# Optimization experiments

Measured on AMD Instinct MI355X. Metric: run time of the kernel, lower is better.

## Reference

```python
import jax, jax.numpy as jnp
import numpy as np

B, A, H, L = 4096, 4096, 768, 4  # batch, num_atoms, hidden_dim, antecedent_len


def setup_inputs() -> dict:
    key = jax.random.key(0)
    ks = jax.random.split(key, 10)
    s = 0.02
    cls = jax.random.normal(ks[0], (B, H), jnp.float32)
    x_ = jax.random.bernoulli(ks[1], 0.5, (B, A)).astype(jnp.float32)
    gru_w_ih = jax.random.normal(ks[2], (3 * H, H), jnp.float32) * s
    gru_w_hh = jax.random.normal(ks[3], (3 * H, H), jnp.float32) * s
    gru_b_ih = jax.random.normal(ks[4], (3 * H,), jnp.float32) * s
    gru_b_hh = jax.random.normal(ks[5], (3 * H,), jnp.float32) * s
    head_w = jax.random.normal(ks[6], (A, H), jnp.float32) * s
    head_b = jax.random.normal(ks[7], (A,), jnp.float32) * s
    ae_weight = jax.random.normal(ks[8], (A, H), jnp.float32) * s
    return {"cls": cls, "x_": x_, "gru_w_ih": gru_w_ih, "gru_w_hh": gru_w_hh,
            "gru_b_ih": gru_b_ih, "gru_b_hh": gru_b_hh, "head_w": head_w,
            "head_b": head_b, "ae_weight": ae_weight}


def _gru_step(x, h, w_ih, w_hh, b_ih, b_hh):
    # torch GRU gate order: r, z, n
    gi = x @ w_ih.T + b_ih          # [B, 3H]
    gh = h @ w_hh.T + b_hh
    i_r, i_z, i_n = jnp.split(gi, 3, axis=-1)
    h_r, h_z, h_n = jnp.split(gh, 3, axis=-1)
    r = jax.nn.sigmoid(i_r + h_r)
    z = jax.nn.sigmoid(i_z + h_z)
    n = jnp.tanh(i_n + r * h_n)
    return (1.0 - z) * n + z * h


def reference(cls, x_, gru_w_ih, gru_w_hh, gru_b_ih, gru_b_hh, head_w, head_b, ae_weight):
    key = jax.random.key(42)
    mask = x_
    h = jnp.zeros_like(cls)
    cur_input = cls
    max_index = None
    rows = jnp.arange(B)
    probs = []
    for j in range(L):
        h = _gru_step(cur_input, h, gru_w_ih, gru_w_hh, gru_b_ih, gru_b_hh)
        out = h @ head_w.T + head_b  # [B, A]  (dropout = identity in eval)
        # filtered_softmax mask update (mutations persist across steps)
        if j == 0:
            empty = jnp.sum(mask, axis=-1) == 0.0
            mask = mask.at[:, 0].set(jnp.where(empty, 1.0, mask[:, 0]))
        else:
            mask = jnp.where((max_index == 0)[:, None], 0.0, mask)
            mask = mask.at[:, 0].set(1.0)
        logits = jnp.where(mask > 0, out, -jnp.inf)
        # hard gumbel-softmax, tau=1 (straight-through)
        key, sub = jax.random.split(key)
        g = jax.random.gumbel(sub, logits.shape, logits.dtype)
        y_soft = jax.nn.softmax(logits + g, axis=1)
        idx = jnp.argmax(y_soft, axis=1)
        y_hard = jax.nn.one_hot(idx, A, dtype=y_soft.dtype)
        prob = y_hard + y_soft - jax.lax.stop_gradient(y_soft)
        max_index = idx
        # scatter zeros at the selected atom (remove from candidate set)
        mask = mask.at[rows, idx].set(0.0)
        probs.append(prob)
        atom_wsum = prob @ jax.lax.stop_gradient(ae_weight)  # [B, H]
        cur_input = cls + atom_wsum
    return jnp.stack(probs, axis=1)  # [B, L, A]
```

## Files before the change

kernel.cpp:

```cpp
#include <hip/hip_runtime.h>
#include <cstdint>
#include <cstddef>
#include <math.h>


#define KB 4096
#define KA 4096
#define KH 768
#define KL 4

typedef __attribute__((ext_vector_type(8))) short bf16x8;
typedef __attribute__((ext_vector_type(4))) float f32x4;

__host__ __device__ inline unsigned rotl32(unsigned x, int d) {
  return (x << d) | (x >> (32 - d));
}

__host__ __device__ inline void tf2x32(unsigned k0, unsigned k1,
                                       unsigned x0, unsigned x1,
                                       unsigned& o0, unsigned& o1) {
  unsigned ks2 = k0 ^ k1 ^ 0x1BD11BDAu;
  x0 += k0; x1 += k1;
#define TF_R(r) { x0 += x1; x1 = rotl32(x1, (r)); x1 ^= x0; }
  TF_R(13) TF_R(15) TF_R(26) TF_R(6)
  x0 += k1;  x1 += ks2 + 1u;
  TF_R(17) TF_R(29) TF_R(16) TF_R(24)
  x0 += ks2; x1 += k0 + 2u;
  TF_R(13) TF_R(15) TF_R(26) TF_R(6)
  x0 += k0;  x1 += k1 + 3u;
  TF_R(17) TF_R(29) TF_R(16) TF_R(24)
  x0 += k1;  x1 += ks2 + 4u;
  TF_R(13) TF_R(15) TF_R(26) TF_R(6)
  x0 += ks2; x1 += k0 + 5u;
#undef TF_R
  o0 = x0; o1 = x1;
}

__device__ inline ushort f2bf(float f) {
  unsigned u = __float_as_uint(f);
  unsigned r = (u + 0x7fffu + ((u >> 16) & 1u)) >> 16;
  return (ushort)r;
}
__device__ inline float bf2f(ushort h) {
  return __uint_as_float(((unsigned)h) << 16);
}

__device__ inline float gumbel_at(unsigned s0, unsigned s1, unsigned ctr) {
  unsigned o0, o1;
  tf2x32(s0, s1, 0u, ctr, o0, o1);
  unsigned bits = o0 ^ o1;
  float f = __uint_as_float((bits >> 9) | 0x3f800000u) - 1.0f;
  const float TINY = 1.17549435e-38f;
  float u = fmaxf(TINY, f + TINY);
  return -logf(-logf(u));
}

__global__ __launch_bounds__(256) void gemm3_nt(
    const ushort* __restrict__ Ahi, const ushort* __restrict__ Alo,
    const ushort* __restrict__ Bhi, const ushort* __restrict__ Blo,
    float* __restrict__ C, long long ldc) {
  __shared__ ushort smem[4 * 128 * 64];
  const int tid = threadIdx.x;
  const int wave = tid >> 6;
  const int lane = tid & 63;
  const long long bm = (long long)blockIdx.y * 128;
  const long long bn = (long long)blockIdx.x * 128;
  const int wm = (wave & 1) * 64;
  const int wn = (wave >> 1) * 64;

  f32x4 acc[4][4];
#pragma unroll
  for (int i = 0; i < 4; ++i)
#pragma unroll
    for (int j = 0; j < 4; ++j) acc[i][j] = (f32x4){0.f, 0.f, 0.f, 0.f};

  const int r = lane >> 3;
  const int csrc = (lane & 7) ^ r;
  const int m15 = lane & 15;
  const int kg = (lane >> 4) & 3;

  for (int kt = 0; kt < 12; ++kt) {
    const int k0 = kt * 64;
#pragma unroll
    for (int s = 0; s < 4; ++s) {
      const int m0 = wave * 32 + s * 8;
      const long long arow = (bm + m0 + r) * KH + k0 + csrc * 8;
      const long long brow = (bn + m0 + r) * KH + k0 + csrc * 8;
      __builtin_amdgcn_global_load_lds(
          (const __attribute__((address_space(1))) void*)(Ahi + arow),
          (__attribute__((address_space(3))) void*)&smem[0 * 8192 + m0 * 64], 16, 0, 0);
      __builtin_amdgcn_global_load_lds(
          (const __attribute__((address_space(1))) void*)(Alo + arow),
          (__attribute__((address_space(3))) void*)&smem[1 * 8192 + m0 * 64], 16, 0, 0);
      __builtin_amdgcn_global_load_lds(
          (const __attribute__((address_space(1))) void*)(Bhi + brow),
          (__attribute__((address_space(3))) void*)&smem[2 * 8192 + m0 * 64], 16, 0, 0);
      __builtin_amdgcn_global_load_lds(
          (const __attribute__((address_space(1))) void*)(Blo + brow),
          (__attribute__((address_space(3))) void*)&smem[3 * 8192 + m0 * 64], 16, 0, 0);
    }
    __syncthreads();
#pragma unroll
    for (int ks = 0; ks < 2; ++ks) {
      bf16x8 ah[4], al[4], bh[4], bl[4];
#pragma unroll
      for (int i = 0; i < 4; ++i) {
        const int m = wm + i * 16 + m15;
        const int slot = (ks * 4 + kg) ^ (lane & 7);
        ah[i] = *(const bf16x8*)&smem[0 * 8192 + m * 64 + slot * 8];
        al[i] = *(const bf16x8*)&smem[1 * 8192 + m * 64 + slot * 8];
        const int n = wn + i * 16 + m15;
        bh[i] = *(const bf16x8*)&smem[2 * 8192 + n * 64 + slot * 8];
        bl[i] = *(const bf16x8*)&smem[3 * 8192 + n * 64 + slot * 8];
      }
#pragma unroll
      for (int i = 0; i < 4; ++i)
#pragma unroll
        for (int j = 0; j < 4; ++j) {
          acc[i][j] = __builtin_amdgcn_mfma_f32_16x16x32_bf16(ah[i], bh[j], acc[i][j], 0, 0, 0);
          acc[i][j] = __builtin_amdgcn_mfma_f32_16x16x32_bf16(ah[i], bl[j], acc[i][j], 0, 0, 0);
          acc[i][j] = __builtin_amdgcn_mfma_f32_16x16x32_bf16(al[i], bh[j], acc[i][j], 0, 0, 0);
        }
    }
    __syncthreads();
  }
  const int rq = (lane >> 4) * 4;
#pragma unroll
  for (int i = 0; i < 4; ++i)
#pragma unroll
    for (int j = 0; j < 4; ++j) {
      const long long n = bn + wn + j * 16 + m15;
#pragma unroll
      for (int rg = 0; rg < 4; ++rg) {
        const long long m = bm + wm + i * 16 + rq + rg;
        C[m * ldc + n] = acc[i][j][rg];
      }
    }
}

__global__ __launch_bounds__(256) void gemm1_nt(
    const ushort* __restrict__ Ahi, const ushort* __restrict__ Bhi,
    float* __restrict__ C, long long ldc) {
  __shared__ ushort smem[2 * 128 * 64];
  const int tid = threadIdx.x;
  const int wave = tid >> 6;
  const int lane = tid & 63;
  const long long bm = (long long)blockIdx.y * 128;
  const long long bn = (long long)blockIdx.x * 128;
  const int wm = (wave & 1) * 64;
  const int wn = (wave >> 1) * 64;

  f32x4 acc[4][4];
#pragma unroll
  for (int i = 0; i < 4; ++i)
#pragma unroll
    for (int j = 0; j < 4; ++j) acc[i][j] = (f32x4){0.f, 0.f, 0.f, 0.f};

  const int r = lane >> 3;
  const int csrc = (lane & 7) ^ r;
  const int m15 = lane & 15;
  const int kg = (lane >> 4) & 3;

  for (int kt = 0; kt < 12; ++kt) {
    const int k0 = kt * 64;
#pragma unroll
    for (int s = 0; s < 4; ++s) {
      const int m0 = wave * 32 + s * 8;
      const long long arow = (bm + m0 + r) * KH + k0 + csrc * 8;
      const long long brow = (bn + m0 + r) * KH + k0 + csrc * 8;
      __builtin_amdgcn_global_load_lds(
          (const __attribute__((address_space(1))) void*)(Ahi + arow),
          (__attribute__((address_space(3))) void*)&smem[0 * 8192 + m0 * 64], 16, 0, 0);
      __builtin_amdgcn_global_load_lds(
          (const __attribute__((address_space(1))) void*)(Bhi + brow),
          (__attribute__((address_space(3))) void*)&smem[1 * 8192 + m0 * 64], 16, 0, 0);
    }
    __syncthreads();
#pragma unroll
    for (int ks = 0; ks < 2; ++ks) {
      bf16x8 ah[4], bh[4];
#pragma unroll
      for (int i = 0; i < 4; ++i) {
        const int m = wm + i * 16 + m15;
        const int slot = (ks * 4 + kg) ^ (lane & 7);
        ah[i] = *(const bf16x8*)&smem[0 * 8192 + m * 64 + slot * 8];
        const int n = wn + i * 16 + m15;
        bh[i] = *(const bf16x8*)&smem[1 * 8192 + n * 64 + slot * 8];
      }
#pragma unroll
      for (int i = 0; i < 4; ++i)
#pragma unroll
        for (int j = 0; j < 4; ++j)
          acc[i][j] = __builtin_amdgcn_mfma_f32_16x16x32_bf16(ah[i], bh[j], acc[i][j], 0, 0, 0);
    }
    __syncthreads();
  }
  const int rq = (lane >> 4) * 4;
#pragma unroll
  for (int i = 0; i < 4; ++i)
#pragma unroll
    for (int j = 0; j < 4; ++j) {
      const long long n = bn + wn + j * 16 + m15;
#pragma unroll
      for (int rg = 0; rg < 4; ++rg) {
        const long long m = bm + wm + i * 16 + rq + rg;
        C[m * ldc + n] = acc[i][j][rg];
      }
    }
}

#define CUM1 442368
#define CUM2 884736
#define CUM3 1671168
#define CUM4 2457600
#define CUM5 3244032
#define PREP_CONV_BLOCKS 12672

__global__ void prep(const float* __restrict__ w_ih, const float* __restrict__ w_hh,
                     const float* __restrict__ head_w, const float* __restrict__ cls,
                     const float* __restrict__ ae_w,
                     ushort* __restrict__ WihHi, ushort* __restrict__ WihLo,
                     ushort* __restrict__ WhhHi, ushort* __restrict__ WhhLo,
                     ushort* __restrict__ HwHi, ushort* __restrict__ CAhi,
                     ushort* __restrict__ CAlo) {
  const int i = blockIdx.x * 256 + threadIdx.x;
  const float* src; ushort* dhi; ushort* dlo; int base; int split; int ofs = 0;
  if (i < CUM1)      { src = w_ih;   dhi = WihHi; dlo = WihLo; base = 0;    split = 1; }
  else if (i < CUM2) { src = w_hh;   dhi = WhhHi; dlo = WhhLo; base = CUM1; split = 1; }
  else if (i < CUM3) { src = head_w; dhi = HwHi;  dlo = 0;     base = CUM2; split = 0; }
  else if (i < CUM4) { src = cls;    dhi = CAhi;  dlo = CAlo;  base = CUM3; split = 1; }
  else               { src = ae_w;   dhi = CAhi;  dlo = CAlo;  base = CUM4; split = 1; ofs = 786432; }
  const int k = i - base;
  float4 v = ((const float4*)src)[k];
  ushort4 h;
  h.x = f2bf(v.x); h.y = f2bf(v.y); h.z = f2bf(v.z); h.w = f2bf(v.w);
  ((ushort4*)dhi)[ofs + k] = h;
  if (split) {
    ushort4 l;
    l.x = f2bf(v.x - bf2f(h.x)); l.y = f2bf(v.y - bf2f(h.y));
    l.z = f2bf(v.z - bf2f(h.z)); l.w = f2bf(v.w - bf2f(h.w));
    ((ushort4*)dlo)[ofs + k] = l;
  }
}

__global__ void gru_gate2(const float* __restrict__ PAE, const float* __restrict__ Gh,
                          const int* __restrict__ idxbuf,
                          const float* __restrict__ b_ih, const float* __restrict__ b_hh,
                          float* __restrict__ h, ushort* __restrict__ hHi,
                          ushort* __restrict__ hLo, int first) {
  int i = blockIdx.x * 256 + threadIdx.x;
  int b = i / KH, c = i - b * KH;
  const float* gp = PAE + (size_t)b * (3 * KH);
  float ir = gp[c], iz = gp[c + KH], in_ = gp[c + 2 * KH];
  float hr = b_hh[c], hz = b_hh[c + KH], hn = b_hh[c + 2 * KH];
  float hp = 0.f;
  if (!first) {
    const float* ga = PAE + ((size_t)KB + idxbuf[b]) * (3 * KH);
    ir += ga[c]; iz += ga[c + KH]; in_ += ga[c + 2 * KH];
    const float* gh = Gh + (size_t)b * (3 * KH);
    hr += gh[c]; hz += gh[c + KH]; hn += gh[c + 2 * KH];
    hp = h[i];
  }
  ir += b_ih[c]; iz += b_ih[c + KH]; in_ += b_ih[c + 2 * KH];
  float rr = 1.f / (1.f + expf(-(ir + hr)));
  float z = 1.f / (1.f + expf(-(iz + hz)));
  float n = tanhf(in_ + rr * hn);
  float hv = (1.f - z) * n + z * hp;
  h[i] = hv;
  ushort hh = f2bf(hv);
  hHi[i] = hh;
  hLo[i] = f2bf(hv - bf2f(hh));
}

__global__ __launch_bounds__(256) void sample_step(
    float* __restrict__ out, const float* __restrict__ head_b,
    const float* __restrict__ x_, unsigned char* __restrict__ mask,
    int* __restrict__ idxbuf, const float* __restrict__ hbuf,
    const float* __restrict__ head_w, int j, unsigned s0, unsigned s1) {
  const int b = blockIdx.x;
  const int tid = threadIdx.x;
  float* orow = out + ((size_t)b * KL + j) * KA;
  unsigned char* mrow = mask + (size_t)b * KA;
  const float* xrow = x_ + (size_t)b * KA;
  __shared__ float sv[256];
  __shared__ int si[256];
  __shared__ int scand[16];
  __shared__ float srefined[16];
  __shared__ int scnt;
  __shared__ int ssel;
  const float EPS = 0.01f;

  if (tid == 0) scnt = 0;

  int idx_prev = 0;
  if (j > 0) idx_prev = idxbuf[b];

  int empty = 0;
  if (j == 0) {
    int cnt = 0;
#pragma unroll
    for (int t = 0; t < 16; ++t) cnt += (xrow[tid + (t << 8)] != 0.f) ? 1 : 0;
    si[tid] = cnt;
    __syncthreads();
    for (int s = 128; s > 0; s >>= 1) {
      if (tid < s) si[tid] += si[tid + s];
      __syncthreads();
    }
    empty = (si[0] == 0);
    __syncthreads();
  }

  float vreg[16];
  unsigned mbits = 0;
  float lmax = -INFINITY;
#pragma unroll
  for (int t = 0; t < 16; ++t) {
    int a = tid + (t << 8);
    int m;
    if (j == 0) {
      m = (xrow[a] != 0.f) ? 1 : 0;
      if (empty && a == 0) m = 1;
    } else {
      m = mrow[a];
      if (idx_prev == 0) m = 0;
      if (a == 0) m = 1;
    }
    float v = -INFINITY;
    if (m) {
      float g = gumbel_at(s0, s1, (unsigned)(b * KA + a));
      v = orow[a] + head_b[a] + g;
      mbits |= (1u << t);
    }
    vreg[t] = v;
    lmax = fmaxf(lmax, v);
  }
  sv[tid] = lmax;
  __syncthreads();
  for (int s = 128; s > 0; s >>= 1) {
    if (tid < s) sv[tid] = fmaxf(sv[tid], sv[tid + s]);
    __syncthreads();
  }
  const float vmax = sv[0];

  const float thresh = vmax - EPS;
#pragma unroll
  for (int t = 0; t < 16; ++t) {
    if (vreg[t] >= thresh) {
      int slot = atomicAdd(&scnt, 1);
      if (slot < 16) scand[slot] = tid + (t << 8);
    }
  }
  __syncthreads();
  const int ncand = min(scnt, 16);

  {
    const int wv = tid >> 6;
    const int lane = tid & 63;
    const float4* h4 = (const float4*)(hbuf + (size_t)b * KH);
    for (int t = wv; t < ncand; t += 4) {
      const int a = scand[t];
      const float4* w4 = (const float4*)(head_w + (size_t)a * KH);
      float sum = 0.f;
#pragma unroll
      for (int u = 0; u < 3; ++u) {
        float4 hv = h4[lane + u * 64];
        float4 wv4 = w4[lane + u * 64];
        sum = fmaf(hv.x, wv4.x, sum);
        sum = fmaf(hv.y, wv4.y, sum);
        sum = fmaf(hv.z, wv4.z, sum);
        sum = fmaf(hv.w, wv4.w, sum);
      }
#pragma unroll
      for (int off = 32; off > 0; off >>= 1) sum += __shfl_down(sum, off);
      if (lane == 0) {
        float g = gumbel_at(s0, s1, (unsigned)(b * KA + a));
        srefined[t] = sum + head_b[a] + g;
      }
    }
  }
  __syncthreads();

  if (tid == 0) {
    float best = -INFINITY;
    int bsel = KA;
    for (int t = 0; t < ncand; ++t) {
      float v = srefined[t];
      int a = scand[t];
      if (v > best || (v == best && a < bsel)) { best = v; bsel = a; }
    }
    ssel = bsel;
  }
  __syncthreads();
  const int sel = ssel;

#pragma unroll
  for (int t = 0; t < 16; ++t) {
    int a = tid + (t << 8);
    int m = (mbits >> t) & 1;
    if (a == sel) m = 0;
    mrow[a] = (unsigned char)m;
    orow[a] = (a == sel) ? 1.f : 0.f;
  }
  if (tid == 0) idxbuf[b] = sel;
}

extern "C" void kernel_launch(void* const* d_in, const int* in_sizes, int n_in,
                              void* d_out, int out_size, void* d_ws, size_t ws_size,
                              hipStream_t stream) {
  const float* cls    = (const float*)d_in[0];
  const float* x_     = (const float*)d_in[1];
  const float* w_ih   = (const float*)d_in[2];
  const float* w_hh   = (const float*)d_in[3];
  const float* b_ih   = (const float*)d_in[4];
  const float* b_hh   = (const float*)d_in[5];
  const float* head_w = (const float*)d_in[6];
  const float* head_b = (const float*)d_in[7];
  const float* ae_w   = (const float*)d_in[8];
  float* out = (float*)d_out;

  char* p = (char*)d_ws;
  ushort* CAhi  = (ushort*)p; p += (size_t)2 * KB * KH * 2;
  ushort* CAlo  = (ushort*)p; p += (size_t)2 * KB * KH * 2;
  ushort* WihHi = (ushort*)p; p += (size_t)3 * KH * KH * 2;
  ushort* WihLo = (ushort*)p; p += (size_t)3 * KH * KH * 2;
  ushort* WhhHi = (ushort*)p; p += (size_t)3 * KH * KH * 2;
  ushort* WhhLo = (ushort*)p; p += (size_t)3 * KH * KH * 2;
  ushort* HwHi  = (ushort*)p; p += (size_t)KA * KH * 2;
  ushort* hHi   = (ushort*)p; p += (size_t)KB * KH * 2;
  ushort* hLo   = (ushort*)p; p += (size_t)KB * KH * 2;
  float*  hbuf  = (float*)p;  p += (size_t)KB * KH * 4;
  float*  PAE   = (float*)p;  p += (size_t)2 * KB * 3 * KH * 4;
  float*  Gh    = (float*)p;  p += (size_t)KB * 3 * KH * 4;
  unsigned char* mask = (unsigned char*)p; p += (size_t)KB * KA;
  int* idxbuf = (int*)p; p += (size_t)KB * 4;

  unsigned key0 = 0u, key1 = 42u;
  unsigned sub0[KL], sub1[KL];
  for (int j = 0; j < KL; ++j) {
    unsigned n0, n1, t0, t1;
    tf2x32(key0, key1, 0u, 0u, n0, n1);
    tf2x32(key0, key1, 0u, 1u, t0, t1);
    sub0[j] = t0; sub1[j] = t1;
    key0 = n0; key1 = n1;
  }

  prep<<<PREP_CONV_BLOCKS, 256, 0, stream>>>(
      w_ih, w_hh, head_w, cls, ae_w,
      WihHi, WihLo, WhhHi, WhhLo, HwHi, CAhi, CAlo);
  gemm3_nt<<<dim3(3 * KH / 128, 2 * KB / 128), 256, 0, stream>>>(
      CAhi, CAlo, WihHi, WihLo, PAE, 3 * KH);

  for (int j = 0; j < KL; ++j) {
    if (j > 0)
      gemm3_nt<<<dim3(3 * KH / 128, KB / 128), 256, 0, stream>>>(
          hHi, hLo, WhhHi, WhhLo, Gh, 3 * KH);
    gru_gate2<<<KB * KH / 256, 256, 0, stream>>>(PAE, Gh, idxbuf, b_ih, b_hh,
                                                 hbuf, hHi, hLo, j == 0);
    gemm1_nt<<<dim3(KA / 128, KB / 128), 256, 0, stream>>>(
        hHi, HwHi, out + (size_t)j * KA, (long long)KL * KA);
    sample_step<<<KB, 256, 0, stream>>>(out, head_b, x_, mask, idxbuf, hbuf,
                                        head_w, j, sub0[j], sub1[j]);
  }
}
```

Baseline: 1.154 ms.

## Halve GEMM K-tile, vectorize GRU gate and sampler, move empty-row check to prep

The GEMM kernels now use a K tile of 32 instead of 64, with a new XOR swizzle. This halves LDS use, which may allow more blocks per CU, but doubles the number of barrier iterations. Register pressure drops because only B fragments are held while A is loaded per row. The GRU gate kernel and the sampling kernel now use float4 and packed-byte vectorized accesses. The per-row empty-mask reduction moves out of the step-0 sampler into extra blocks of the prep kernel.

After: 1.055 ms. -8.6%, faster.

```diff
diff --git a/kernel.cpp b/kernel.cpp
--- a/kernel.cpp
+++ b/kernel.cpp
@@ -55,11 +55,16 @@
   return -logf(-logf(u));
 }
 
+#define GLDS(gp, lp) \
+  __builtin_amdgcn_global_load_lds( \
+      (const __attribute__((address_space(1))) void*)(gp), \
+      (__attribute__((address_space(3))) void*)(lp), 16, 0, 0)
+
 __global__ __launch_bounds__(256) void gemm3_nt(
     const ushort* __restrict__ Ahi, const ushort* __restrict__ Alo,
     const ushort* __restrict__ Bhi, const ushort* __restrict__ Blo,
     float* __restrict__ C, long long ldc) {
-  __shared__ ushort smem[4 * 128 * 64];
+  __shared__ ushort smem[4 * 128 * 32];
   const int tid = threadIdx.x;
   const int wave = tid >> 6;
   const int lane = tid & 63;
@@ -74,53 +79,44 @@
 #pragma unroll
     for (int j = 0; j < 4; ++j) acc[i][j] = (f32x4){0.f, 0.f, 0.f, 0.f};
 
-  const int r = lane >> 3;
-  const int csrc = (lane & 7) ^ r;
+  const int r = lane >> 2;
+  const int cs = lane & 3;
+  const int csrc = cs ^ ((r & 3) ^ ((r >> 2) & 3));
   const int m15 = lane & 15;
   const int kg = (lane >> 4) & 3;
-
-  for (int kt = 0; kt < 12; ++kt) {
-    const int k0 = kt * 64;
-#pragma unroll
-    for (int s = 0; s < 4; ++s) {
-      const int m0 = wave * 32 + s * 8;
+  const int slot = kg ^ ((m15 & 3) ^ ((m15 >> 2) & 3));
+
+  for (int kt = 0; kt < 24; ++kt) {
+    const int k0 = kt * 32;
+#pragma unroll
+    for (int s = 0; s < 2; ++s) {
+      const int m0 = wave * 32 + s * 16;
       const long long arow = (bm + m0 + r) * KH + k0 + csrc * 8;
       const long long brow = (bn + m0 + r) * KH + k0 + csrc * 8;
-      __builtin_amdgcn_global_load_lds(
-          (const __attribute__((address_space(1))) void*)(Ahi + arow),
-          (__attribute__((address_space(3))) void*)&smem[0 * 8192 + m0 * 64], 16, 0, 0);
-      __builtin_amdgcn_global_load_lds(
-          (const __attribute__((address_space(1))) void*)(Alo + arow),
-          (__attribute__((address_space(3))) void*)&smem[1 * 8192 + m0 * 64], 16, 0, 0);
-      __builtin_amdgcn_global_load_lds(
-          (const __attribute__((address_space(1))) void*)(Bhi + brow),
-          (__attribute__((address_space(3))) void*)&smem[2 * 8192 + m0 * 64], 16, 0, 0);
-      __builtin_amdgcn_global_load_lds(
-          (const __attribute__((address_space(1))) void*)(Blo + brow),
-          (__attribute__((address_space(3))) void*)&smem[3 * 8192 + m0 * 64], 16, 0, 0);
+      GLDS(Ahi + arow, &smem[0 * 4096 + m0 * 32]);
+      GLDS(Alo + arow, &smem[1 * 4096 + m0 * 32]);
+      GLDS(Bhi + brow, &smem[2 * 4096 + m0 * 32]);
+      GLDS(Blo + brow, &smem[3 * 4096 + m0 * 32]);
     }
     __syncthreads();
-#pragma unroll
-    for (int ks = 0; ks < 2; ++ks) {
-      bf16x8 ah[4], al[4], bh[4], bl[4];
-#pragma unroll
-      for (int i = 0; i < 4; ++i) {
-        const int m = wm + i * 16 + m15;
-        const int slot = (ks * 4 + kg) ^ (lane & 7);
-        ah[i] = *(const bf16x8*)&smem[0 * 8192 + m * 64 + slot * 8];
-        al[i] = *(const bf16x8*)&smem[1 * 8192 + m * 64 + slot * 8];
-        const int n = wn + i * 16 + m15;
-        bh[i] = *(const bf16x8*)&smem[2 * 8192 + n * 64 + slot * 8];
-        bl[i] = *(const bf16x8*)&smem[3 * 8192 + n * 64 + slot * 8];
-      }
-#pragma unroll
-      for (int i = 0; i < 4; ++i)
-#pragma unroll
-        for (int j = 0; j < 4; ++j) {
-          acc[i][j] = __builtin_amdgcn_mfma_f32_16x16x32_bf16(ah[i], bh[j], acc[i][j], 0, 0, 0);
-          acc[i][j] = __builtin_amdgcn_mfma_f32_16x16x32_bf16(ah[i], bl[j], acc[i][j], 0, 0, 0);
-          acc[i][j] = __builtin_amdgcn_mfma_f32_16x16x32_bf16(al[i], bh[j], acc[i][j], 0, 0, 0);
-        }
+    bf16x8 bh[4], bl[4];
+#pragma unroll
+    for (int jj = 0; jj < 4; ++jj) {
+      const int n = wn + jj * 16 + m15;
+      bh[jj] = *(const bf16x8*)&smem[2 * 4096 + n * 32 + slot * 8];
+      bl[jj] = *(const bf16x8*)&smem[3 * 4096 + n * 32 + slot * 8];
+    }
+#pragma unroll
+    for (int i = 0; i < 4; ++i) {
+      const int m = wm + i * 16 + m15;
+      bf16x8 ah = *(const bf16x8*)&smem[0 * 4096 + m * 32 + slot * 8];
+      bf16x8 al = *(const bf16x8*)&smem[1 * 4096 + m * 32 + slot * 8];
+#pragma unroll
+      for (int jj = 0; jj < 4; ++jj) {
+        acc[i][jj] = __builtin_amdgcn_mfma_f32_16x16x32_bf16(ah, bh[jj], acc[i][jj], 0, 0, 0);
+        acc[i][jj] = __builtin_amdgcn_mfma_f32_16x16x32_bf16(ah, bl[jj], acc[i][jj], 0, 0, 0);
+        acc[i][jj] = __builtin_amdgcn_mfma_f32_16x16x32_bf16(al, bh[jj], acc[i][jj], 0, 0, 0);
+      }
     }
     __syncthreads();
   }
@@ -141,7 +137,7 @@
 __global__ __launch_bounds__(256) void gemm1_nt(
     const ushort* __restrict__ Ahi, const ushort* __restrict__ Bhi,
     float* __restrict__ C, long long ldc) {
-  __shared__ ushort smem[2 * 128 * 64];
+  __shared__ ushort smem[2 * 128 * 32];
   const int tid = threadIdx.x;
   const int wave = tid >> 6;
   const int lane = tid & 63;
@@ -156,42 +152,37 @@
 #pragma unroll
     for (int j = 0; j < 4; ++j) acc[i][j] = (f32x4){0.f, 0.f, 0.f, 0.f};
 
-  const int r = lane >> 3;
-  const int csrc = (lane & 7) ^ r;
+  const int r = lane >> 2;
+  const int cs = lane & 3;
+  const int csrc = cs ^ ((r & 3) ^ ((r >> 2) & 3));
   const int m15 = lane & 15;
   const int kg = (lane >> 4) & 3;
-
-  for (int kt = 0; kt < 12; ++kt) {
-    const int k0 = kt * 64;
-#pragma unroll
-    for (int s = 0; s < 4; ++s) {
-      const int m0 = wave * 32 + s * 8;
+  const int slot = kg ^ ((m15 & 3) ^ ((m15 >> 2) & 3));
+
+  for (int kt = 0; kt < 24; ++kt) {
+    const int k0 = kt * 32;
+#pragma unroll
+    for (int s = 0; s < 2; ++s) {
+      const int m0 = wave * 32 + s * 16;
       const long long arow = (bm + m0 + r) * KH + k0 + csrc * 8;
       const long long brow = (bn + m0 + r) * KH + k0 + csrc * 8;
-      __builtin_amdgcn_global_load_lds(
-          (const __attribute__((address_space(1))) void*)(Ahi + arow),
-          (__attribute__((address_space(3))) void*)&smem[0 * 8192 + m0 * 64], 16, 0, 0);
-      __builtin_amdgcn_global_load_lds(
-          (const __attribute__((address_space(1))) void*)(Bhi + brow),
-          (__attribute__((address_space(3))) void*)&smem[1 * 8192 + m0 * 64], 16, 0, 0);
+      GLDS(Ahi + arow, &smem[0 * 4096 + m0 * 32]);
+      GLDS(Bhi + brow, &smem[1 * 4096 + m0 * 32]);
     }
     __syncthreads();
-#pragma unroll
-    for (int ks = 0; ks < 2; ++ks) {
-      bf16x8 ah[4], bh[4];
-#pragma unroll
-      for (int i = 0; i < 4; ++i) {
-        const int m = wm + i * 16 + m15;
-        const int slot = (ks * 4 + kg) ^ (lane & 7);
-        ah[i] = *(const bf16x8*)&smem[0 * 8192 + m * 64 + slot * 8];
-        const int n = wn + i * 16 + m15;
-        bh[i] = *(const bf16x8*)&smem[1 * 8192 + n * 64 + slot * 8];
-      }
-#pragma unroll
-      for (int i = 0; i < 4; ++i)
-#pragma unroll
-        for (int j = 0; j < 4; ++j)
-          acc[i][j] = __builtin_amdgcn_mfma_f32_16x16x32_bf16(ah[i], bh[j], acc[i][j], 0, 0, 0);
+    bf16x8 bh[4];
+#pragma unroll
+    for (int jj = 0; jj < 4; ++jj) {
+      const int n = wn + jj * 16 + m15;
+      bh[jj] = *(const bf16x8*)&smem[1 * 4096 + n * 32 + slot * 8];
+    }
+#pragma unroll
+    for (int i = 0; i < 4; ++i) {
+      const int m = wm + i * 16 + m15;
+      bf16x8 ah = *(const bf16x8*)&smem[0 * 4096 + m * 32 + slot * 8];
+#pragma unroll
+      for (int jj = 0; jj < 4; ++jj)
+        acc[i][jj] = __builtin_amdgcn_mfma_f32_16x16x32_bf16(ah, bh[jj], acc[i][jj], 0, 0, 0);
     }
     __syncthreads();
   }
@@ -218,28 +209,49 @@
 
 __global__ void prep(const float* __restrict__ w_ih, const float* __restrict__ w_hh,
                      const float* __restrict__ head_w, const float* __restrict__ cls,
-                     const float* __restrict__ ae_w,
+                     const float* __restrict__ ae_w, const float* __restrict__ x_,
                      ushort* __restrict__ WihHi, ushort* __restrict__ WihLo,
                      ushort* __restrict__ WhhHi, ushort* __restrict__ WhhLo,
                      ushort* __restrict__ HwHi, ushort* __restrict__ CAhi,
-                     ushort* __restrict__ CAlo) {
-  const int i = blockIdx.x * 256 + threadIdx.x;
-  const float* src; ushort* dhi; ushort* dlo; int base; int split; int ofs = 0;
-  if (i < CUM1)      { src = w_ih;   dhi = WihHi; dlo = WihLo; base = 0;    split = 1; }
-  else if (i < CUM2) { src = w_hh;   dhi = WhhHi; dlo = WhhLo; base = CUM1; split = 1; }
-  else if (i < CUM3) { src = head_w; dhi = HwHi;  dlo = 0;     base = CUM2; split = 0; }
-  else if (i < CUM4) { src = cls;    dhi = CAhi;  dlo = CAlo;  base = CUM3; split = 1; }
-  else               { src = ae_w;   dhi = CAhi;  dlo = CAlo;  base = CUM4; split = 1; ofs = 786432; }
-  const int k = i - base;
-  float4 v = ((const float4*)src)[k];
-  ushort4 h;
-  h.x = f2bf(v.x); h.y = f2bf(v.y); h.z = f2bf(v.z); h.w = f2bf(v.w);
-  ((ushort4*)dhi)[ofs + k] = h;
-  if (split) {
-    ushort4 l;
-    l.x = f2bf(v.x - bf2f(h.x)); l.y = f2bf(v.y - bf2f(h.y));
-    l.z = f2bf(v.z - bf2f(h.z)); l.w = f2bf(v.w - bf2f(h.w));
-    ((ushort4*)dlo)[ofs + k] = l;
+                     ushort* __restrict__ CAlo, unsigned char* __restrict__ empty) {
+  const int blk = blockIdx.x;
+  const int tid = threadIdx.x;
+  if (blk < PREP_CONV_BLOCKS) {
+    const int i = blk * 256 + tid;
+    const float* src; ushort* dhi; ushort* dlo; int base; int split; int ofs = 0;
+    if (i < CUM1)      { src = w_ih;   dhi = WihHi; dlo = WihLo; base = 0;    split = 1; }
+    else if (i < CUM2) { src = w_hh;   dhi = WhhHi; dlo = WhhLo; base = CUM1; split = 1; }
+    else if (i < CUM3) { src = head_w; dhi = HwHi;  dlo = 0;     base = CUM2; split = 0; }
+    else if (i < CUM4) { src = cls;    dhi = CAhi;  dlo = CAlo;  base = CUM3; split = 1; }
+    else               { src = ae_w;   dhi = CAhi;  dlo = CAlo;  base = CUM4; split = 1; ofs = 786432; }
+    const int k = i - base;
+    float4 v = ((const float4*)src)[k];
+    ushort4 h;
+    h.x = f2bf(v.x); h.y = f2bf(v.y); h.z = f2bf(v.z); h.w = f2bf(v.w);
+    ((ushort4*)dhi)[ofs + k] = h;
+    if (split) {
+      ushort4 l;
+      l.x = f2bf(v.x - bf2f(h.x)); l.y = f2bf(v.y - bf2f(h.y));
+      l.z = f2bf(v.z - bf2f(h.z)); l.w = f2bf(v.w - bf2f(h.w));
+      ((ushort4*)dlo)[ofs + k] = l;
+    }
+  } else {
+    const int row = blk - PREP_CONV_BLOCKS;
+    __shared__ int scnt[256];
+    const float4* xr = (const float4*)(x_ + (size_t)row * KA);
+    int cnt = 0;
+#pragma unroll
+    for (int k = 0; k < 4; ++k) {
+      float4 v = xr[tid + (k << 8)];
+      cnt += (v.x != 0.f) + (v.y != 0.f) + (v.z != 0.f) + (v.w != 0.f);
+    }
+    scnt[tid] = cnt;
+    __syncthreads();
+    for (int s = 128; s > 0; s >>= 1) {
+      if (tid < s) scnt[tid] += scnt[tid + s];
+      __syncthreads();
+    }
+    if (tid == 0) empty[row] = (scnt[0] == 0) ? 1 : 0;
   }
 }
 
@@ -248,42 +260,55 @@
                           const float* __restrict__ b_ih, const float* __restrict__ b_hh,
                           float* __restrict__ h, ushort* __restrict__ hHi,
                           ushort* __restrict__ hLo, int first) {
-  int i = blockIdx.x * 256 + threadIdx.x;
-  int b = i / KH, c = i - b * KH;
-  const float* gp = PAE + (size_t)b * (3 * KH);
-  float ir = gp[c], iz = gp[c + KH], in_ = gp[c + 2 * KH];
-  float hr = b_hh[c], hz = b_hh[c + KH], hn = b_hh[c + 2 * KH];
-  float hp = 0.f;
+  int i4 = blockIdx.x * 256 + threadIdx.x;
+  int b = i4 / (KH / 4);
+  int c4 = i4 - b * (KH / 4);
+  const f32x4* gp = (const f32x4*)(PAE + (size_t)b * (3 * KH));
+  f32x4 ir = gp[c4], iz = gp[c4 + 192], inn = gp[c4 + 384];
+  const f32x4* bi = (const f32x4*)b_ih;
+  const f32x4* bhh = (const f32x4*)b_hh;
+  f32x4 hr = bhh[c4], hz = bhh[c4 + 192], hn = bhh[c4 + 384];
+  f32x4 hp = (f32x4){0.f, 0.f, 0.f, 0.f};
   if (!first) {
-    const float* ga = PAE + ((size_t)KB + idxbuf[b]) * (3 * KH);
-    ir += ga[c]; iz += ga[c + KH]; in_ += ga[c + 2 * KH];
-    const float* gh = Gh + (size_t)b * (3 * KH);
-    hr += gh[c]; hz += gh[c + KH]; hn += gh[c + 2 * KH];
-    hp = h[i];
-  }
-  ir += b_ih[c]; iz += b_ih[c + KH]; in_ += b_ih[c + 2 * KH];
-  float rr = 1.f / (1.f + expf(-(ir + hr)));
-  float z = 1.f / (1.f + expf(-(iz + hz)));
-  float n = tanhf(in_ + rr * hn);
-  float hv = (1.f - z) * n + z * hp;
-  h[i] = hv;
-  ushort hh = f2bf(hv);
-  hHi[i] = hh;
-  hLo[i] = f2bf(hv - bf2f(hh));
+    const f32x4* ga = (const f32x4*)(PAE + ((size_t)KB + idxbuf[b]) * (3 * KH));
+    ir += ga[c4]; iz += ga[c4 + 192]; inn += ga[c4 + 384];
+    const f32x4* gh = (const f32x4*)(Gh + (size_t)b * (3 * KH));
+    hr += gh[c4]; hz += gh[c4 + 192]; hn += gh[c4 + 384];
+    hp = ((const f32x4*)h)[i4];
+  }
+  ir += bi[c4]; iz += bi[c4 + 192]; inn += bi[c4 + 384];
+  f32x4 hv;
+  ushort4 hh, hl;
+  ushort* hhp = &hh.x;
+  ushort* hlp = &hl.x;
+#pragma unroll
+  for (int e = 0; e < 4; ++e) {
+    float rr = 1.f / (1.f + expf(-(ir[e] + hr[e])));
+    float z = 1.f / (1.f + expf(-(iz[e] + hz[e])));
+    float n = tanhf(inn[e] + rr * hn[e]);
+    float v = (1.f - z) * n + z * hp[e];
+    hv[e] = v;
+    ushort hb = f2bf(v);
+    hhp[e] = hb;
+    hlp[e] = f2bf(v - bf2f(hb));
+  }
+  ((f32x4*)h)[i4] = hv;
+  ((ushort4*)hHi)[i4] = hh;
+  ((ushort4*)hLo)[i4] = hl;
 }
 
 __global__ __launch_bounds__(256) void sample_step(
     float* __restrict__ out, const float* __restrict__ head_b,
     const float* __restrict__ x_, unsigned char* __restrict__ mask,
     int* __restrict__ idxbuf, const float* __restrict__ hbuf,
-    const float* __restrict__ head_w, int j, unsigned s0, unsigned s1) {
+    const float* __restrict__ head_w, const unsigned char* __restrict__ empty,
+    int j, unsigned s0, unsigned s1) {
   const int b = blockIdx.x;
   const int tid = threadIdx.x;
   float* orow = out + ((size_t)b * KL + j) * KA;
   unsigned char* mrow = mask + (size_t)b * KA;
   const float* xrow = x_ + (size_t)b * KA;
   __shared__ float sv[256];
-  __shared__ int si[256];
   __shared__ int scand[16];
   __shared__ float srefined[16];
   __shared__ int scnt;
@@ -292,47 +317,49 @@
 
   if (tid == 0) scnt = 0;
 
-  int idx_prev = 0;
-  if (j > 0) idx_prev = idxbuf[b];
-
-  int empty = 0;
-  if (j == 0) {
-    int cnt = 0;
-#pragma unroll
-    for (int t = 0; t < 16; ++t) cnt += (xrow[tid + (t << 8)] != 0.f) ? 1 : 0;
-    si[tid] = cnt;
-    __syncthreads();
-    for (int s = 128; s > 0; s >>= 1) {
-      if (tid < s) si[tid] += si[tid + s];
-      __syncthreads();
-    }
-    empty = (si[0] == 0);
-    __syncthreads();
-  }
+  const int idx_prev = (j > 0) ? idxbuf[b] : 0;
+  const int emp = (j == 0) ? empty[b] : 0;
 
   float vreg[16];
   unsigned mbits = 0;
   float lmax = -INFINITY;
-#pragma unroll
-  for (int t = 0; t < 16; ++t) {
-    int a = tid + (t << 8);
-    int m;
+  const float4* orow4 = (const float4*)orow;
+  const float4* xrow4 = (const float4*)xrow;
+  const unsigned* mrow4 = (const unsigned*)mrow;
+  const float4* hb4 = (const float4*)head_b;
+#pragma unroll
+  for (int k = 0; k < 4; ++k) {
+    const int ci = tid + (k << 8);
+    const int abase = ci * 4;
+    float4 lv = orow4[ci];
+    float4 hbv = hb4[ci];
+    float lvv[4] = {lv.x + hbv.x, lv.y + hbv.y, lv.z + hbv.z, lv.w + hbv.w};
+    float xvv[4] = {0.f, 0.f, 0.f, 0.f};
+    unsigned mword = 0;
     if (j == 0) {
-      m = (xrow[a] != 0.f) ? 1 : 0;
-      if (empty && a == 0) m = 1;
+      float4 xv = xrow4[ci];
+      xvv[0] = xv.x; xvv[1] = xv.y; xvv[2] = xv.z; xvv[3] = xv.w;
     } else {
-      m = mrow[a];
-      if (idx_prev == 0) m = 0;
-      if (a == 0) m = 1;
-    }
-    float v = -INFINITY;
-    if (m) {
-      float g = gumbel_at(s0, s1, (unsigned)(b * KA + a));
-      v = orow[a] + head_b[a] + g;
-      mbits |= (1u << t);
-    }
-    vreg[t] = v;
-    lmax = fmaxf(lmax, v);
+      mword = mrow4[ci];
+    }
+#pragma unroll
+    for (int e = 0; e < 4; ++e) {
+      const int a = abase + e;
+      int m;
+      if (j == 0) {
+        m = (xvv[e] != 0.f) || (emp && a == 0);
+      } else {
+        m = (a == 0) || (idx_prev != 0 && ((mword >> (8 * e)) & 0xffu));
+      }
+      float v = -INFINITY;
+      if (m) {
+        float g = gumbel_at(s0, s1, (unsigned)(b * KA + a));
+        v = lvv[e] + g;
+        mbits |= (1u << (k * 4 + e));
+      }
+      vreg[k * 4 + e] = v;
+      lmax = fmaxf(lmax, v);
+    }
   }
   sv[tid] = lmax;
   __syncthreads();
@@ -344,12 +371,14 @@
 
   const float thresh = vmax - EPS;
 #pragma unroll
-  for (int t = 0; t < 16; ++t) {
-    if (vreg[t] >= thresh) {
-      int slot = atomicAdd(&scnt, 1);
-      if (slot < 16) scand[slot] = tid + (t << 8);
-    }
-  }
+  for (int k = 0; k < 4; ++k)
+#pragma unroll
+    for (int e = 0; e < 4; ++e) {
+      if (vreg[k * 4 + e] >= thresh) {
+        int slot = atomicAdd(&scnt, 1);
+        if (slot < 16) scand[slot] = (tid + (k << 8)) * 4 + e;
+      }
+    }
   __syncthreads();
   const int ncand = min(scnt, 16);
 
@@ -394,12 +423,22 @@
   const int sel = ssel;
 
 #pragma unroll
-  for (int t = 0; t < 16; ++t) {
-    int a = tid + (t << 8);
-    int m = (mbits >> t) & 1;
-    if (a == sel) m = 0;
-    mrow[a] = (unsigned char)m;
-    orow[a] = (a == sel) ? 1.f : 0.f;
+  for (int k = 0; k < 4; ++k) {
+    const int ci = tid + (k << 8);
+    const int abase = ci * 4;
+    unsigned mw = 0;
+    float4 ov;
+    float* ovp = &ov.x;
+#pragma unroll
+    for (int e = 0; e < 4; ++e) {
+      const int a = abase + e;
+      int m = (mbits >> (k * 4 + e)) & 1;
+      if (a == sel) m = 0;
+      mw |= ((unsigned)m) << (8 * e);
+      ovp[e] = (a == sel) ? 1.f : 0.f;
+    }
+    ((unsigned*)mrow)[ci] = mw;
+    ((float4*)orow)[ci] = ov;
   }
   if (tid == 0) idxbuf[b] = sel;
 }
@@ -431,7 +470,8 @@
   float*  hbuf  = (float*)p;  p += (size_t)KB * KH * 4;
   float*  PAE   = (float*)p;  p += (size_t)2 * KB * 3 * KH * 4;
   float*  Gh    = (float*)p;  p += (size_t)KB * 3 * KH * 4;
-  unsigned char* mask = (unsigned char*)p; p += (size_t)KB * KA;
+  unsigned char* mask  = (unsigned char*)p; p += (size_t)KB * KA;
+  unsigned char* empty = (unsigned char*)p; p += (size_t)KB;
   int* idxbuf = (int*)p; p += (size_t)KB * 4;
 
   unsigned key0 = 0u, key1 = 42u;
@@ -444,9 +484,9 @@
     key0 = n0; key1 = n1;
   }
 
-  prep<<<PREP_CONV_BLOCKS, 256, 0, stream>>>(
-      w_ih, w_hh, head_w, cls, ae_w,
-      WihHi, WihLo, WhhHi, WhhLo, HwHi, CAhi, CAlo);
+  prep<<<PREP_CONV_BLOCKS + KB, 256, 0, stream>>>(
+      w_ih, w_hh, head_w, cls, ae_w, x_,
+      WihHi, WihLo, WhhHi, WhhLo, HwHi, CAhi, CAlo, empty);
   gemm3_nt<<<dim3(3 * KH / 128, 2 * KB / 128), 256, 0, stream>>>(
       CAhi, CAlo, WihHi, WihLo, PAE, 3 * KH);
 
@@ -454,11 +494,11 @@
     if (j > 0)
       gemm3_nt<<<dim3(3 * KH / 128, KB / 128), 256, 0, stream>>>(
           hHi, hLo, WhhHi, WhhLo, Gh, 3 * KH);
-    gru_gate2<<<KB * KH / 256, 256, 0, stream>>>(PAE, Gh, idxbuf, b_ih, b_hh,
-                                                 hbuf, hHi, hLo, j == 0);
+    gru_gate2<<<KB * KH / 4 / 256, 256, 0, stream>>>(PAE, Gh, idxbuf, b_ih, b_hh,
+                                                     hbuf, hHi, hLo, j == 0);
     gemm1_nt<<<dim3(KA / 128, KB / 128), 256, 0, stream>>>(
         hHi, HwHi, out + (size_t)j * KA, (long long)KL * KA);
     sample_step<<<KB, 256, 0, stream>>>(out, head_b, x_, mask, idxbuf, hbuf,
-                                        head_w, j, sub0[j], sub1[j]);
-  }
-}
+                                        head_w, empty, j, sub0[j], sub1[j]);
+  }
+}
```
